# Performance work log

Measured on AMD Instinct MI355X. Metric: run time of the kernel, lower is better.

Reference implementation:

```python
import jax, jax.numpy as jnp
import numpy as np

N = 8192  # number of nodes (input_size[0])
K = 32    # number of archetypes


def setup_inputs() -> dict:
    key = jax.random.key(0)
    kA, kb, ka, kX, kC = jax.random.split(key, 5)
    A = (jax.random.uniform(kA, (N, N)) < 0.05).astype(jnp.float32)
    beta = jax.random.normal(kb, (N,), dtype=jnp.float32)
    a = jax.random.normal(ka, (1,), dtype=jnp.float32)
    X = jax.random.normal(kX, (K, N), dtype=jnp.float32)
    C = jax.random.normal(kC, (N, K), dtype=jnp.float32)
    return {"A": A, "beta": beta, "a": a, "X": X, "C": C}


def reference(A, beta, a, X, C):
    # z_dist[i,j] = (X[:,i]-X[:,j])^T C_s^T K C_s (X[:,i]-X[:,j]),
    # with K = softmax(X)^T softmax(X), C_s = softmax(C) (both column-softmax, dim=0).
    Xs = jax.nn.softmax(X, axis=0)          # (K, N)
    Cs = jax.nn.softmax(C, axis=0)          # (N, K)
    E = Xs @ Cs                             # (K, K) = softmax(X) @ softmax(C)
    M = E.T @ E                             # (K, K) = Cs^T Xs^T Xs Cs, PSD
    # quadratic form over all pairs via G = X^T M X (raw X columns, as in the torch loop)
    G = X.T @ (M @ X)                       # (N, N)
    q = jnp.diagonal(G)                     # (N,) = x_i^T M x_i
    z_dist = q[:, None] + q[None, :] - 2.0 * G
    theta = beta[:, None] + beta[None, :] - a * z_dist  # (N, N)
    sp = jax.nn.softplus(theta)
    LL = 0.5 * jnp.sum(theta * A) - 0.5 * (jnp.sum(sp) - jnp.sum(jnp.diagonal(sp)))
    return LL
```

## Files before the change

kernel.cpp:

```cpp
#include <hip/hip_runtime.h>
#include <hip/hip_bf16.h>

#define NN 8192
#define KK 32

__device__ __forceinline__ float wave_reduce_sum(float v) {
    #pragma unroll
    for (int off = 32; off > 0; off >>= 1) v += __shfl_down(v, off);
    return v;
}
__device__ __forceinline__ float wave_reduce_max(float v) {
    #pragma unroll
    for (int off = 32; off > 0; off >>= 1) v = fmaxf(v, __shfl_down(v, off));
    return v;
}

__global__ void kc_colstats(const float* __restrict__ C, float* __restrict__ mC,
                            float* __restrict__ sC) {
    const int l = blockIdx.x;
    const int t = threadIdx.x;
    __shared__ float wmax[4], wsum[4];

    float m = -INFINITY;
    for (int u = 0; u < NN / 256; ++u)
        m = fmaxf(m, C[(size_t)(u * 256 + t) * KK + l]);
    m = wave_reduce_max(m);
    if ((t & 63) == 0) wmax[t >> 6] = m;
    __syncthreads();
    const float mm = fmaxf(fmaxf(wmax[0], wmax[1]), fmaxf(wmax[2], wmax[3]));

    float s = 0.f;
    for (int u = 0; u < NN / 256; ++u)
        s += __expf(C[(size_t)(u * 256 + t) * KK + l] - mm);
    s = wave_reduce_sum(s);
    if ((t & 63) == 0) wsum[t >> 6] = s;
    __syncthreads();
    if (t == 0) {
        mC[l] = mm;
        sC[l] = wsum[0] + wsum[1] + wsum[2] + wsum[3];
    }
}

__global__ void kx_softmax(const float* __restrict__ X, float* __restrict__ Xs) {
    const int n = blockIdx.x * 256 + threadIdx.x;
    float e[KK];
    float m = -INFINITY;
    #pragma unroll
    for (int k = 0; k < KK; ++k) {
        e[k] = X[(size_t)k * NN + n];
        m = fmaxf(m, e[k]);
    }
    float s = 0.f;
    #pragma unroll
    for (int k = 0; k < KK; ++k) {
        e[k] = __expf(e[k] - m);
        s += e[k];
    }
    const float r = 1.f / s;
    #pragma unroll
    for (int k = 0; k < KK; ++k) Xs[(size_t)k * NN + n] = e[k] * r;
}

__global__ void ke_E(const float* __restrict__ Xs, const float* __restrict__ C,
                     const float* __restrict__ mC, const float* __restrict__ sC,
                     float* __restrict__ E) {
    __shared__ float xsl[KK * 33];
    __shared__ float cql[32 * 33];
    __shared__ float mCl[KK], rsCl[KK];
    const int tid = threadIdx.x;
    if (tid < KK) { mCl[tid] = mC[tid]; rsCl[tid] = 1.f / sC[tid]; }
    const int k = tid & 31, l = tid >> 5;
    const int sk = tid >> 5, sn = tid & 31;
    const int nb0 = blockIdx.x * (NN / 64);
    float acc = 0.f;
    for (int b = 0; b < 4; ++b) {
        const int nb = nb0 + b * 32;
        __syncthreads();
        xsl[sk * 33 + sn] = Xs[(size_t)sk * NN + nb + sn];
        const float cv = C[(size_t)nb * KK + tid];
        cql[(tid >> 5) * 33 + (tid & 31)] =
            __expf(cv - mCl[tid & 31]) * rsCl[tid & 31];
        __syncthreads();
        #pragma unroll
        for (int n = 0; n < 32; ++n)
            acc = fmaf(xsl[k * 33 + n], cql[n * 33 + l], acc);
    }
    atomicAdd(&E[k * KK + l], acc);
}

__global__ void km_M(const float* __restrict__ E, float* __restrict__ M) {
    __shared__ float el[KK * 33];
    const int tid = threadIdx.x;
    el[(tid >> 5) * 33 + (tid & 31)] = E[tid];
    __syncthreads();
    const int l1 = tid & 31, l2 = tid >> 5;
    float acc = 0.f;
    #pragma unroll
    for (int kk = 0; kk < KK; ++kk)
        acc = fmaf(el[kk * 33 + l1], el[kk * 33 + l2], acc);
    M[tid] = acc;
}

__global__ void kp_prep(const float* __restrict__ X, const float* __restrict__ beta,
                        const float* __restrict__ a_ptr, const float* __restrict__ M,
                        float* __restrict__ Xt, float* __restrict__ Wt,
                        float* __restrict__ f, double* __restrict__ acc) {
    __shared__ float Ml[KK * KK];
    const int tid = threadIdx.x;
    #pragma unroll
    for (int u = 0; u < 4; ++u) Ml[tid + 256 * u] = M[tid + 256 * u];
    __syncthreads();
    const int n = blockIdx.x * 256 + tid;
    float x[KK], v[KK];
    #pragma unroll
    for (int k = 0; k < KK; ++k) x[k] = X[(size_t)k * NN + n];
    const float a = a_ptr[0];
    #pragma unroll
    for (int l = 0; l < KK; ++l) {
        float s = 0.f;
        #pragma unroll
        for (int k = 0; k < KK; ++k) s = fmaf(Ml[l * KK + k], x[k], s);
        v[l] = s;
    }
    float q = 0.f;
    #pragma unroll
    for (int l = 0; l < KK; ++l) q = fmaf(x[l], v[l], q);
    const float b = beta[n];
    f[n] = b - a * q;
    const float two_a = 2.f * a;
    #pragma unroll
    for (int k = 0; k < KK; ++k) {
        Xt[(size_t)n * KK + k] = x[k];
        Wt[(size_t)n * KK + k] = two_a * v[k];
    }
    const float th = 2.f * b;
    float sp = fmaxf(th, 0.f) + __logf(1.f + __expf(-fabsf(th)));
    sp = wave_reduce_sum(sp);
    __shared__ float rd[4];
    if ((tid & 63) == 0) rd[tid >> 6] = sp;
    __syncthreads();
    if (tid == 0)
        atomicAdd(&acc[2], (double)rd[0] + rd[1] + rd[2] + rd[3]);
}

#define II 32
#define JPANEL 1024

__global__ __launch_bounds__(256) void kl_main(
    const float* __restrict__ A, const float* __restrict__ Xt,
    const float* __restrict__ Wt, const float* __restrict__ f,
    double* __restrict__ acc) {
    __shared__ float xs[II * KK];
    __shared__ float fi[II];
    const int tid = threadIdx.x;
    const int ibase = blockIdx.y * II;
    const int jpan = blockIdx.x * JPANEL;

    ((float4*)xs)[tid] = ((const float4*)(Xt + (size_t)ibase * KK))[tid];
    if (tid < II) fi[tid] = f[ibase + tid];
    __syncthreads();

    float accA = 0.f, accS = 0.f;

    for (int c = 0; c < JPANEL / 256; ++c) {
        const int jj = jpan + c * 256 + tid;
        const float4* w4 = (const float4*)&Wt[(size_t)jj * KK];
        const float4 w0 = w4[0], w1 = w4[1], w2 = w4[2], w3 = w4[3];
        const float4 w4r = w4[4], w5 = w4[5], w6 = w4[6], w7 = w4[7];
        const float fj = f[jj];

        #pragma unroll 2
        for (int i = 0; i < II; ++i) {
            const float Av = A[(size_t)(ibase + i) * NN + jj];
            const float4* x4 = (const float4*)&xs[i * KK];
            const float4 x0 = x4[0], x1 = x4[1], x2 = x4[2], x3 = x4[3];
            const float4 x4r = x4[4], x5 = x4[5], x6 = x4[6], x7 = x4[7];

            float t0 = x0.x * w0.x, t1 = x0.y * w0.y, t2 = x0.z * w0.z, t3 = x0.w * w0.w;
            t0 = fmaf(x1.x, w1.x, t0); t1 = fmaf(x1.y, w1.y, t1);
            t2 = fmaf(x1.z, w1.z, t2); t3 = fmaf(x1.w, w1.w, t3);
            t0 = fmaf(x2.x, w2.x, t0); t1 = fmaf(x2.y, w2.y, t1);
            t2 = fmaf(x2.z, w2.z, t2); t3 = fmaf(x2.w, w2.w, t3);
            t0 = fmaf(x3.x, w3.x, t0); t1 = fmaf(x3.y, w3.y, t1);
            t2 = fmaf(x3.z, w3.z, t2); t3 = fmaf(x3.w, w3.w, t3);
            t0 = fmaf(x4r.x, w4r.x, t0); t1 = fmaf(x4r.y, w4r.y, t1);
            t2 = fmaf(x4r.z, w4r.z, t2); t3 = fmaf(x4r.w, w4r.w, t3);
            t0 = fmaf(x5.x, w5.x, t0); t1 = fmaf(x5.y, w5.y, t1);
            t2 = fmaf(x5.z, w5.z, t2); t3 = fmaf(x5.w, w5.w, t3);
            t0 = fmaf(x6.x, w6.x, t0); t1 = fmaf(x6.y, w6.y, t1);
            t2 = fmaf(x6.z, w6.z, t2); t3 = fmaf(x6.w, w6.w, t3);
            t0 = fmaf(x7.x, w7.x, t0); t1 = fmaf(x7.y, w7.y, t1);
            t2 = fmaf(x7.z, w7.z, t2); t3 = fmaf(x7.w, w7.w, t3);

            const float th = fi[i] + fj + ((t0 + t1) + (t2 + t3));
            accA = fmaf(th, Av, accA);
            accS += fmaxf(th, 0.f) + __logf(1.f + __expf(-fabsf(th)));
        }
    }

    accA = wave_reduce_sum(accA);
    accS = wave_reduce_sum(accS);
    __shared__ float rA[4], rS[4];
    if ((tid & 63) == 0) { rA[tid >> 6] = accA; rS[tid >> 6] = accS; }
    __syncthreads();
    if (tid == 0) {
        const double dA = (double)rA[0] + rA[1] + rA[2] + rA[3];
        const double dS = (double)rS[0] + rS[1] + rS[2] + rS[3];
        atomicAdd(&acc[0], dA);
        atomicAdd(&acc[1], dS);
    }
}

__global__ void kf_final(const double* __restrict__ acc, float* __restrict__ out) {
    out[0] = (float)(0.5 * (acc[0] - (acc[1] - acc[2])));
}

extern "C" void kernel_launch(void* const* d_in, const int* in_sizes, int n_in,
                              void* d_out, int out_size, void* d_ws, size_t ws_size,
                              hipStream_t stream) {
    const float* Ain    = (const float*)d_in[0];
    const float* betain = (const float*)d_in[1];
    const float* ain    = (const float*)d_in[2];
    const float* Xin    = (const float*)d_in[3];
    const float* Cin    = (const float*)d_in[4];
    float* out = (float*)d_out;

    char* ws = (char*)d_ws;
    float*  E   = (float*)(ws + 0);
    double* acc = (double*)(ws + 4096);
    float*  mC  = (float*)(ws + 4160);
    float*  sC  = (float*)(ws + 4288);
    float*  M   = (float*)(ws + 4608);
    float*  f   = (float*)(ws + 8704);
    float*  Xs  = (float*)(ws + 65536);
    float*  Xt  = (float*)(ws + 65536 + 1048576);
    float*  Wt  = (float*)(ws + 65536 + 2097152);

    hipMemsetAsync(ws, 0, 4128, stream);

    kc_colstats<<<KK, 256, 0, stream>>>(Cin, mC, sC);
    kx_softmax<<<NN / 256, 256, 0, stream>>>(Xin, Xs);
    ke_E<<<64, 1024, 0, stream>>>(Xs, Cin, mC, sC, E);
    km_M<<<1, 1024, 0, stream>>>(E, M);
    kp_prep<<<NN / 256, 256, 0, stream>>>(Xin, betain, ain, M, Xt, Wt, f, acc);
    kl_main<<<dim3(NN / JPANEL, NN / II), 256, 0, stream>>>(Ain, Xt, Wt, f, acc);
    kf_final<<<1, 1, 0, stream>>>(acc, out);
}
```

Measured before the change: 490.1 us.

## Split likelihood into A-GEMM and MFMA softplus passes with bf16 hi/lo splitting

Rewrites the theta*A term algebraically: sum_ij A_ij*theta_ij becomes A @ [W | 1 | f], computed with bf16 MFMA GEMMs using hi/lo splits of W, followed by a per-row reduction with X and f. The softplus sum is computed in a separate set of waves, using three bf16 MFMAs (hi*hi, hi*lo, lo*hi) to approximate the fp32 dot products. Both parts are fused into one heterogeneous kernel and finished by a new reduction kernel. The A values are rounded to bf16, which is exact for binary input, and the precision split risks small accuracy loss. It adds large partial-sum buffers and extra launches.

```diff
diff --git a/kernel.cpp b/kernel.cpp
--- a/kernel.cpp
+++ b/kernel.cpp
@@ -4,6 +4,9 @@
 #define NN 8192
 #define KK 32
 
+typedef __attribute__((ext_vector_type(8))) short short8v;
+typedef __attribute__((ext_vector_type(4))) float float4v;
+
 __device__ __forceinline__ float wave_reduce_sum(float v) {
     #pragma unroll
     for (int off = 32; off > 0; off >>= 1) v += __shfl_down(v, off);
@@ -13,6 +16,13 @@
     #pragma unroll
     for (int off = 32; off > 0; off >>= 1) v = fmaxf(v, __shfl_down(v, off));
     return v;
+}
+__device__ __forceinline__ unsigned short f2bf(float x) {
+    unsigned int u = __float_as_uint(x);
+    return (unsigned short)((u + 0x7fffu + ((u >> 16) & 1u)) >> 16);
+}
+__device__ __forceinline__ float bf2f(unsigned short h) {
+    return __uint_as_float(((unsigned int)h) << 16);
 }
 
 __global__ void kc_colstats(const float* __restrict__ C, float* __restrict__ mC,
@@ -102,112 +112,185 @@
 }
 
 __global__ void kp_prep(const float* __restrict__ X, const float* __restrict__ beta,
-                        const float* __restrict__ a_ptr, const float* __restrict__ M,
-                        float* __restrict__ Xt, float* __restrict__ Wt,
-                        float* __restrict__ f, double* __restrict__ acc) {
+                        const float* __restrict__ a_ptr, const float* __restrict__ Mm,
+                        float* __restrict__ Xt, float* __restrict__ f,
+                        unsigned short* __restrict__ Xh, unsigned short* __restrict__ Xl,
+                        unsigned short* __restrict__ Wh, unsigned short* __restrict__ Wl,
+                        unsigned short* __restrict__ Bh, unsigned short* __restrict__ Bl,
+                        double* __restrict__ acc) {
     __shared__ float Ml[KK * KK];
     const int tid = threadIdx.x;
     #pragma unroll
-    for (int u = 0; u < 4; ++u) Ml[tid + 256 * u] = M[tid + 256 * u];
+    for (int u = 0; u < 4; ++u) Ml[tid + 256 * u] = Mm[tid + 256 * u];
     __syncthreads();
     const int n = blockIdx.x * 256 + tid;
     float x[KK], v[KK];
     #pragma unroll
     for (int k = 0; k < KK; ++k) x[k] = X[(size_t)k * NN + n];
     const float a = a_ptr[0];
+    const float two_a = 2.f * a;
     #pragma unroll
     for (int l = 0; l < KK; ++l) {
         float s = 0.f;
         #pragma unroll
         for (int k = 0; k < KK; ++k) s = fmaf(Ml[l * KK + k], x[k], s);
-        v[l] = s;
-    }
-    float q = 0.f;
-    #pragma unroll
-    for (int l = 0; l < KK; ++l) q = fmaf(x[l], v[l], q);
+        v[l] = two_a * s;
+    }
+    float q2 = 0.f;
+    #pragma unroll
+    for (int l = 0; l < KK; ++l) q2 = fmaf(x[l], v[l], q2);
     const float b = beta[n];
-    f[n] = b - a * q;
-    const float two_a = 2.f * a;
-    #pragma unroll
-    for (int k = 0; k < KK; ++k) {
-        Xt[(size_t)n * KK + k] = x[k];
-        Wt[(size_t)n * KK + k] = two_a * v[k];
+    const float fn = b - 0.5f * q2;
+    f[n] = fn;
+
+    union PK { unsigned short u[8]; short8v s; };
+    PK xh, xl, wh, wl;
+    #pragma unroll
+    for (int g = 0; g < 4; ++g) {
+        #pragma unroll
+        for (int e = 0; e < 8; ++e) {
+            const int k = g * 8 + e;
+            const float xv = x[k];
+            Xt[(size_t)n * KK + k] = xv;
+            const unsigned short h = f2bf(xv);
+            xh.u[e] = h;
+            xl.u[e] = f2bf(xv - bf2f(h));
+            const float wv = v[k];
+            const unsigned short hw = f2bf(wv);
+            const unsigned short lw = f2bf(wv - bf2f(hw));
+            wh.u[e] = hw;
+            wl.u[e] = lw;
+            Bh[(size_t)k * NN + n] = hw;
+            Bl[(size_t)k * NN + n] = lw;
+        }
+        *(short8v*)&Xh[(size_t)n * KK + g * 8] = xh.s;
+        *(short8v*)&Xl[(size_t)n * KK + g * 8] = xl.s;
+        *(short8v*)&Wh[(size_t)n * KK + g * 8] = wh.s;
+        *(short8v*)&Wl[(size_t)n * KK + g * 8] = wl.s;
+    }
+    Bh[(size_t)32 * NN + n] = 0x3F80; Bl[(size_t)32 * NN + n] = 0;
+    const unsigned short hf = f2bf(fn);
+    Bh[(size_t)33 * NN + n] = hf;
+    Bl[(size_t)33 * NN + n] = f2bf(fn - bf2f(hf));
+    #pragma unroll
+    for (int k = 34; k < 48; ++k) {
+        Bh[(size_t)k * NN + n] = 0;
+        Bl[(size_t)k * NN + n] = 0;
     }
     const float th = 2.f * b;
     float sp = fmaxf(th, 0.f) + __logf(1.f + __expf(-fabsf(th)));
     sp = wave_reduce_sum(sp);
-    __shared__ float rd[4];
-    if ((tid & 63) == 0) rd[tid >> 6] = sp;
-    __syncthreads();
-    if (tid == 0)
-        atomicAdd(&acc[2], (double)rd[0] + rd[1] + rd[2] + rd[3]);
-}
-
-#define II 32
-#define JPANEL 1024
-
-__global__ __launch_bounds__(256) void kl_main(
-    const float* __restrict__ A, const float* __restrict__ Xt,
-    const float* __restrict__ Wt, const float* __restrict__ f,
+    if ((tid & 63) == 0) atomicAdd(&acc[2], (double)sp);
+}
+
+#define GEMM_BLOCKS 1024
+#define GEMM_WAVES  (GEMM_BLOCKS * 4)
+#define SP_BLOCKS   2048
+#define FAT_BLOCKS  (GEMM_BLOCKS + SP_BLOCKS)
+
+__global__ __launch_bounds__(256) void k_fat(
+    const float* __restrict__ A, const float* __restrict__ f,
+    const unsigned short* __restrict__ Xh, const unsigned short* __restrict__ Xl,
+    const unsigned short* __restrict__ Wh, const unsigned short* __restrict__ Wl,
+    const unsigned short* __restrict__ Bh, const unsigned short* __restrict__ Bl,
+    float* __restrict__ Ppart, float* __restrict__ Ssc) {
+    const int tid  = threadIdx.x;
+    const int lane = tid & 63;
+    const int l15  = lane & 15;
+    const int klo  = (lane >> 4) << 3;
+    const int wid  = blockIdx.x * 4 + (tid >> 6);
+
+    if (blockIdx.x < GEMM_BLOCKS) {
+        const int ibase = (wid >> 3) << 4;
+        const int chunk = wid & 7;
+        float4v c0 = {0.f, 0.f, 0.f, 0.f}, c1 = c0, c2 = c0;
+        const float* arow = &A[(size_t)(ibase + l15) * NN];
+        #pragma unroll 2
+        for (int s = 0; s < 32; ++s) {
+            const int j0 = (chunk << 10) + (s << 5) + klo;
+            const float4 a0 = *(const float4*)&arow[j0];
+            const float4 a1 = *(const float4*)&arow[j0 + 4];
+            union { unsigned short u[8]; short8v s8; } af;
+            af.u[0] = f2bf(a0.x); af.u[1] = f2bf(a0.y);
+            af.u[2] = f2bf(a0.z); af.u[3] = f2bf(a0.w);
+            af.u[4] = f2bf(a1.x); af.u[5] = f2bf(a1.y);
+            af.u[6] = f2bf(a1.z); af.u[7] = f2bf(a1.w);
+            const size_t bo = (size_t)l15 * NN + j0;
+            short8v b;
+            b = *(const short8v*)&Bh[bo];
+            c0 = __builtin_amdgcn_mfma_f32_16x16x32_bf16(af.s8, b, c0, 0, 0, 0);
+            b = *(const short8v*)&Bl[bo];
+            c0 = __builtin_amdgcn_mfma_f32_16x16x32_bf16(af.s8, b, c0, 0, 0, 0);
+            b = *(const short8v*)&Bh[bo + (size_t)16 * NN];
+            c1 = __builtin_amdgcn_mfma_f32_16x16x32_bf16(af.s8, b, c1, 0, 0, 0);
+            b = *(const short8v*)&Bl[bo + (size_t)16 * NN];
+            c1 = __builtin_amdgcn_mfma_f32_16x16x32_bf16(af.s8, b, c1, 0, 0, 0);
+            b = *(const short8v*)&Bh[bo + (size_t)32 * NN];
+            c2 = __builtin_amdgcn_mfma_f32_16x16x32_bf16(af.s8, b, c2, 0, 0, 0);
+            b = *(const short8v*)&Bl[bo + (size_t)32 * NN];
+            c2 = __builtin_amdgcn_mfma_f32_16x16x32_bf16(af.s8, b, c2, 0, 0, 0);
+        }
+        const size_t pb = ((size_t)chunk * NN + ibase + ((lane >> 4) << 2)) * 48 + l15;
+        #pragma unroll
+        for (int r = 0; r < 4; ++r) {
+            Ppart[pb + (size_t)r * 48]      = c0[r];
+            Ppart[pb + (size_t)r * 48 + 16] = c1[r];
+            Ppart[pb + (size_t)r * 48 + 32] = c2[r];
+        }
+    } else {
+        const int t = wid - GEMM_WAVES;
+        const int ibase = (t >> 4) << 4;
+        const int jc = (t & 15) << 9;
+        const short8v xh = *(const short8v*)&Xh[(size_t)(ibase + l15) * KK + klo];
+        const short8v xl = *(const short8v*)&Xl[(size_t)(ibase + l15) * KK + klo];
+        float fr[4];
+        #pragma unroll
+        for (int r = 0; r < 4; ++r) fr[r] = f[ibase + ((lane >> 4) << 2) + r];
+        float accS = 0.f;
+        for (int jt = 0; jt < 32; ++jt) {
+            const int jb = jc + (jt << 4);
+            const size_t wo = (size_t)(jb + l15) * KK + klo;
+            const short8v wh = *(const short8v*)&Wh[wo];
+            const short8v wl = *(const short8v*)&Wl[wo];
+            const float fj = f[jb + l15];
+            float4v d = {0.f, 0.f, 0.f, 0.f};
+            d = __builtin_amdgcn_mfma_f32_16x16x32_bf16(xl, wh, d, 0, 0, 0);
+            d = __builtin_amdgcn_mfma_f32_16x16x32_bf16(xh, wl, d, 0, 0, 0);
+            d = __builtin_amdgcn_mfma_f32_16x16x32_bf16(xh, wh, d, 0, 0, 0);
+            #pragma unroll
+            for (int r = 0; r < 4; ++r) {
+                const float th = fr[r] + fj + d[r];
+                accS += fmaxf(th, 0.f) + __logf(1.f + __expf(-fabsf(th)));
+            }
+        }
+        accS = wave_reduce_sum(accS);
+        if (lane == 0) Ssc[t] = accS;
+    }
+}
+
+__global__ __launch_bounds__(256) void kr_reduce(
+    const float* __restrict__ Ppart, const float* __restrict__ Xt,
+    const float* __restrict__ f, const float* __restrict__ Ssc,
     double* __restrict__ acc) {
-    __shared__ float xs[II * KK];
-    __shared__ float fi[II];
-    const int tid = threadIdx.x;
-    const int ibase = blockIdx.y * II;
-    const int jpan = blockIdx.x * JPANEL;
-
-    ((float4*)xs)[tid] = ((const float4*)(Xt + (size_t)ibase * KK))[tid];
-    if (tid < II) fi[tid] = f[ibase + tid];
-    __syncthreads();
-
-    float accA = 0.f, accS = 0.f;
-
-    for (int c = 0; c < JPANEL / 256; ++c) {
-        const int jj = jpan + c * 256 + tid;
-        const float4* w4 = (const float4*)&Wt[(size_t)jj * KK];
-        const float4 w0 = w4[0], w1 = w4[1], w2 = w4[2], w3 = w4[3];
-        const float4 w4r = w4[4], w5 = w4[5], w6 = w4[6], w7 = w4[7];
-        const float fj = f[jj];
-
-        #pragma unroll 2
-        for (int i = 0; i < II; ++i) {
-            const float Av = A[(size_t)(ibase + i) * NN + jj];
-            const float4* x4 = (const float4*)&xs[i * KK];
-            const float4 x0 = x4[0], x1 = x4[1], x2 = x4[2], x3 = x4[3];
-            const float4 x4r = x4[4], x5 = x4[5], x6 = x4[6], x7 = x4[7];
-
-            float t0 = x0.x * w0.x, t1 = x0.y * w0.y, t2 = x0.z * w0.z, t3 = x0.w * w0.w;
-            t0 = fmaf(x1.x, w1.x, t0); t1 = fmaf(x1.y, w1.y, t1);
-            t2 = fmaf(x1.z, w1.z, t2); t3 = fmaf(x1.w, w1.w, t3);
-            t0 = fmaf(x2.x, w2.x, t0); t1 = fmaf(x2.y, w2.y, t1);
-            t2 = fmaf(x2.z, w2.z, t2); t3 = fmaf(x2.w, w2.w, t3);
-            t0 = fmaf(x3.x, w3.x, t0); t1 = fmaf(x3.y, w3.y, t1);
-            t2 = fmaf(x3.z, w3.z, t2); t3 = fmaf(x3.w, w3.w, t3);
-            t0 = fmaf(x4r.x, w4r.x, t0); t1 = fmaf(x4r.y, w4r.y, t1);
-            t2 = fmaf(x4r.z, w4r.z, t2); t3 = fmaf(x4r.w, w4r.w, t3);
-            t0 = fmaf(x5.x, w5.x, t0); t1 = fmaf(x5.y, w5.y, t1);
-            t2 = fmaf(x5.z, w5.z, t2); t3 = fmaf(x5.w, w5.w, t3);
-            t0 = fmaf(x6.x, w6.x, t0); t1 = fmaf(x6.y, w6.y, t1);
-            t2 = fmaf(x6.z, w6.z, t2); t3 = fmaf(x6.w, w6.w, t3);
-            t0 = fmaf(x7.x, w7.x, t0); t1 = fmaf(x7.y, w7.y, t1);
-            t2 = fmaf(x7.z, w7.z, t2); t3 = fmaf(x7.w, w7.w, t3);
-
-            const float th = fi[i] + fj + ((t0 + t1) + (t2 + t3));
-            accA = fmaf(th, Av, accA);
-            accS += fmaxf(th, 0.f) + __logf(1.f + __expf(-fabsf(th)));
-        }
-    }
-
-    accA = wave_reduce_sum(accA);
-    accS = wave_reduce_sum(accS);
-    __shared__ float rA[4], rS[4];
-    if ((tid & 63) == 0) { rA[tid >> 6] = accA; rS[tid >> 6] = accS; }
-    __syncthreads();
-    if (tid == 0) {
-        const double dA = (double)rA[0] + rA[1] + rA[2] + rA[3];
-        const double dS = (double)rS[0] + rS[1] + rS[2] + rS[3];
-        atomicAdd(&acc[0], dA);
-        atomicAdd(&acc[1], dS);
+    const int i = blockIdx.x * 256 + threadIdx.x;
+    float ps[48];
+    #pragma unroll
+    for (int q = 0; q < 48; ++q) ps[q] = 0.f;
+    for (int c = 0; c < 8; ++c) {
+        const float* pp = &Ppart[((size_t)c * NN + i) * 48];
+        #pragma unroll
+        for (int q = 0; q < 48; ++q) ps[q] += pp[q];
+    }
+    const float* xt = &Xt[(size_t)i * KK];
+    float s = 0.f;
+    #pragma unroll
+    for (int k = 0; k < KK; ++k) s = fmaf(xt[k], ps[k], s);
+    s += f[i] * ps[32] + ps[33];
+    const float sA = wave_reduce_sum(s);
+    const float sS = wave_reduce_sum(Ssc[i]);
+    if ((threadIdx.x & 63) == 0) {
+        atomicAdd(&acc[0], (double)sA);
+        atomicAdd(&acc[1], (double)sS);
     }
 }
 
@@ -226,15 +309,22 @@
     float* out = (float*)d_out;
 
     char* ws = (char*)d_ws;
-    float*  E   = (float*)(ws + 0);
-    double* acc = (double*)(ws + 4096);
-    float*  mC  = (float*)(ws + 4160);
-    float*  sC  = (float*)(ws + 4288);
-    float*  M   = (float*)(ws + 4608);
-    float*  f   = (float*)(ws + 8704);
-    float*  Xs  = (float*)(ws + 65536);
-    float*  Xt  = (float*)(ws + 65536 + 1048576);
-    float*  Wt  = (float*)(ws + 65536 + 2097152);
+    float*          E   = (float*)(ws + 0);
+    double*         acc = (double*)(ws + 4096);
+    float*          mC  = (float*)(ws + 4160);
+    float*          sC  = (float*)(ws + 4288);
+    float*          M   = (float*)(ws + 4608);
+    float*          f   = (float*)(ws + 8704);
+    float*          Xt  = (float*)(ws + 65536);
+    unsigned short* Xh  = (unsigned short*)(ws + 1114112);
+    unsigned short* Xl  = (unsigned short*)(ws + 1638400);
+    unsigned short* Wh  = (unsigned short*)(ws + 2162688);
+    unsigned short* Wl  = (unsigned short*)(ws + 2686976);
+    unsigned short* Bh  = (unsigned short*)(ws + 3211264);
+    unsigned short* Bl  = (unsigned short*)(ws + 3997696);
+    float*          Pp  = (float*)(ws + 4784128);
+    float*          Ssc = (float*)(ws + 17367040);
+    float*          Xs  = (float*)(ws + 17399808);
 
     hipMemsetAsync(ws, 0, 4128, stream);
 
@@ -242,7 +332,9 @@
     kx_softmax<<<NN / 256, 256, 0, stream>>>(Xin, Xs);
     ke_E<<<64, 1024, 0, stream>>>(Xs, Cin, mC, sC, E);
     km_M<<<1, 1024, 0, stream>>>(E, M);
-    kp_prep<<<NN / 256, 256, 0, stream>>>(Xin, betain, ain, M, Xt, Wt, f, acc);
-    kl_main<<<dim3(NN / JPANEL, NN / II), 256, 0, stream>>>(Ain, Xt, Wt, f, acc);
+    kp_prep<<<NN / 256, 256, 0, stream>>>(Xin, betain, ain, M, Xt, f,
+                                          Xh, Xl, Wh, Wl, Bh, Bl, acc);
+    k_fat<<<FAT_BLOCKS, 256, 0, stream>>>(Ain, f, Xh, Xl, Wh, Wl, Bh, Bl, Pp, Ssc);
+    kr_reduce<<<NN / 256, 256, 0, stream>>>(Pp, Xt, f, Ssc, acc);
     kf_final<<<1, 1, 0, stream>>>(acc, out);
 }
```

Result: slower. 517.7 us (+5.6%).
